# Kernel tuning notes

Hardware: AMD Instinct MI355X
Metric: run time of the kernel (lower is better)

Reference implementation:

```python
import jax, jax.numpy as jnp
import numpy as np

N_EMBD = 1024
N_HEAD = 16
B, T = 4, 2048
NEG = -1e8  # matches the -100000000.0 additive mask in the torch code


def setup_inputs() -> dict:
    key = jax.random.key(0)
    ks = jax.random.split(key, 6)
    x = jax.random.normal(ks[0], (B, T, N_EMBD), dtype=jnp.float32)
    l = jax.random.randint(ks[1], (B,), 1, T + 1, dtype=jnp.int64 if jax.config.jax_enable_x64 else jnp.int32)
    W_attn = jax.random.normal(ks[2], (N_EMBD, 3 * N_EMBD), dtype=jnp.float32) * 0.02
    b_attn = jnp.zeros((3 * N_EMBD,), dtype=jnp.float32)
    W_proj = jax.random.normal(ks[3], (N_EMBD, N_EMBD), dtype=jnp.float32) * 0.02
    b_proj = jnp.zeros((N_EMBD,), dtype=jnp.float32)
    return {"x": x, "l": l, "W_attn": W_attn, "b_attn": b_attn,
            "W_proj": W_proj, "b_proj": b_proj}


def _build_mask(l, Tdim, dtype):
    # additive mask [B, T, T]: 0 where (q < l_b) & (k < l_b) & (k <= q), else NEG
    idx = jnp.arange(Tdim)
    q_ok = idx[None, :, None] < l[:, None, None]
    k_ok = idx[None, None, :] < l[:, None, None]
    causal = idx[:, None] >= idx[None, :]
    keep = q_ok & k_ok & causal[None]
    return jnp.where(keep, jnp.array(0.0, dtype), jnp.array(NEG, dtype))


def reference(x, l, W_attn, b_attn, W_proj, b_proj):
    Bs, Ts, C = x.shape
    H, D = N_HEAD, C // N_HEAD
    qkv = x @ W_attn + b_attn                              # [B,T,3C]
    q, k, v = jnp.split(qkv, 3, axis=-1)
    q = q.reshape(Bs, Ts, H, D).transpose(0, 2, 1, 3)      # [B,H,T,D]
    k = k.reshape(Bs, Ts, H, D).transpose(0, 2, 1, 3)
    v = v.reshape(Bs, Ts, H, D).transpose(0, 2, 1, 3)
    mask = _build_mask(l, Ts, x.dtype)                     # [B,T,T]
    att = jnp.einsum('bhqd,bhkd->bhqk', q, k) * (1.0 / np.sqrt(D))
    att = att + mask[:, None, :, :]
    att = jax.nn.softmax(att, axis=-1)                     # dropout p=0 -> identity
    y = jnp.einsum('bhqk,bhkd->bhqd', att, v)              # [B,H,T,D]
    y = y.transpose(0, 2, 1, 3).reshape(Bs, Ts, C)
    return y @ W_proj + b_proj
```

## Files before the change

### kernel.cpp

```cpp
#include <hip/hip_runtime.h>

typedef unsigned short UST;
typedef __attribute__((ext_vector_type(8))) short short8;
typedef __attribute__((ext_vector_type(4))) float f32x4;

__device__ __forceinline__ UST f2bf(float f) {
  unsigned int u = __float_as_uint(f);
  u += 0x7FFFu + ((u >> 16) & 1u);
  return (UST)(u >> 16);
}
__device__ __forceinline__ float bf2f(UST u) {
  unsigned int x = ((unsigned int)u) << 16;
  return __uint_as_float(x);
}

__device__ __forceinline__ void gload16(const void* g, void* l) {
  __builtin_amdgcn_global_load_lds((__attribute__((address_space(1))) void*)(g),
                                   (__attribute__((address_space(3))) void*)(l), 16, 0, 0);
}

__global__ __launch_bounds__(256) void k_cvt_bf16(const float* __restrict__ X,
                                                  UST* __restrict__ Y, int n8) {
  int i = blockIdx.x * 256 + threadIdx.x;
  if (i >= n8) return;
  const float4* p = (const float4*)(X + (size_t)i * 8);
  float4 a = p[0], b = p[1];
  short8 o;
  o[0] = (short)f2bf(a.x); o[1] = (short)f2bf(a.y);
  o[2] = (short)f2bf(a.z); o[3] = (short)f2bf(a.w);
  o[4] = (short)f2bf(b.x); o[5] = (short)f2bf(b.y);
  o[6] = (short)f2bf(b.z); o[7] = (short)f2bf(b.w);
  *(short8*)(Y + (size_t)i * 8) = o;
}

__global__ __launch_bounds__(256) void k_transpose_bf16(const float* __restrict__ W,
                                                        UST* __restrict__ WT, int K, int N) {
  __shared__ float tile[64][65];
  int n0 = blockIdx.x * 64, k0 = blockIdx.y * 64;
  int t = threadIdx.x;
#pragma unroll
  for (int p = 0; p < 16; ++p) {
    int e = p * 256 + t;
    tile[e >> 6][e & 63] = W[(size_t)(k0 + (e >> 6)) * N + n0 + (e & 63)];
  }
  __syncthreads();
#pragma unroll
  for (int p = 0; p < 16; ++p) {
    int e = p * 256 + t;
    WT[(size_t)(n0 + (e >> 6)) * K + k0 + (e & 63)] = f2bf(tile[e & 63][e >> 6]);
  }
}

template <int EPI, int GX, int GY>
__global__ __launch_bounds__(256) void k_gemm_bt(const UST* __restrict__ A,
                                                 const UST* __restrict__ Bt,
                                                 const float* __restrict__ bias,
                                                 void* __restrict__ Cout,
                                                 int M, int N, int K) {
  __shared__ __align__(16) UST Alds[128 * 32];
  __shared__ __align__(16) UST Blds[128 * 32];
  const int t = threadIdx.x, lane = t & 63, w = t >> 6;
  const int lr = lane & 15, lg = lane >> 4;
  const int f = blockIdx.x;
  const int cpx = (GX * GY) / 8;
  const int swz = (f & 7) * cpx + (f >> 3);
  const int brow = (swz / GX) * 128, bcol = (swz % GX) * 128;
  const int wr = (w >> 1) * 64, wc = (w & 1) * 64;
  f32x4 acc[4][4] = {};

  for (int k0 = 0; k0 < K; k0 += 32) {
#pragma unroll
    for (int j = 0; j < 2; ++j) {
      int c = j * 256 + t;
      gload16(A + (size_t)(brow + (c >> 2)) * K + k0 + (c & 3) * 8,
              &Alds[(j * 256 + w * 64) * 8]);
      gload16(Bt + (size_t)(bcol + (c >> 2)) * K + k0 + (c & 3) * 8,
              &Blds[(j * 256 + w * 64) * 8]);
    }
    __syncthreads();
    short8 af[4], bf[4];
#pragma unroll
    for (int i = 0; i < 4; ++i) {
      af[i] = *(const short8*)&Alds[(wr + i * 16 + lr) * 32 + lg * 8];
      bf[i] = *(const short8*)&Blds[(wc + i * 16 + lr) * 32 + lg * 8];
    }
#pragma unroll
    for (int mi = 0; mi < 4; ++mi)
#pragma unroll
      for (int ni = 0; ni < 4; ++ni)
        acc[mi][ni] = __builtin_amdgcn_mfma_f32_16x16x32_bf16(af[mi], bf[ni], acc[mi][ni], 0, 0, 0);
    __syncthreads();
  }
#pragma unroll
  for (int ni = 0; ni < 4; ++ni) {
    int n = bcol + wc + ni * 16 + lr;
    float bv = bias[n];
#pragma unroll
    for (int mi = 0; mi < 4; ++mi) {
#pragma unroll
      for (int r = 0; r < 4; ++r) {
        int m = brow + wr + mi * 16 + lg * 4 + r;
        float v = acc[mi][ni][r] + bv;
        if (EPI == 1) ((UST*)Cout)[(size_t)m * N + n] = f2bf(v);
        else          ((float*)Cout)[(size_t)m * N + n] = v;
      }
    }
  }
}

__global__ __launch_bounds__(256) void k_vsum(const UST* __restrict__ qkv,
                                              float* __restrict__ pbuf) {
  const int h = blockIdx.x, b = blockIdx.y, z = blockIdx.z;
  const int t = threadIdx.x;
  const int dgrp = t & 7, kslot = t >> 3;
  const UST* Vg = qkv + (size_t)b * 2048 * 3072 + h * 64 + 2048;
  float acc[8] = {0.f, 0.f, 0.f, 0.f, 0.f, 0.f, 0.f, 0.f};
#pragma unroll
  for (int i = 0; i < 16; ++i) {
    int k = z * 512 + kslot * 16 + i;
    short8 v8 = *(const short8*)&Vg[(size_t)k * 3072 + dgrp * 8];
#pragma unroll
    for (int j = 0; j < 8; ++j) acc[j] += bf2f((UST)v8[j]);
  }
  __shared__ float red[32 * 68];
#pragma unroll
  for (int j = 0; j < 8; ++j) red[kslot * 68 + dgrp * 8 + j] = acc[j];
  __syncthreads();
  if (t < 64) {
    float s = 0.f;
#pragma unroll
    for (int ks = 0; ks < 32; ++ks) s += red[ks * 68 + t];
    pbuf[((size_t)(z * 4 + b) * 16 + h) * 64 + t] = s;
  }
}

__global__ __launch_bounds__(256) void k_attn(const UST* __restrict__ qkv,
                                              const int* __restrict__ L,
                                              const float* __restrict__ pbuf,
                                              UST* __restrict__ Ab) {
  const int qt = blockIdx.x, h = blockIdx.y, b = blockIdx.z;
  const int t = threadIdx.x, lane = t & 63, w = t >> 6;
  const int lr = lane & 15, lg = lane >> 4;
  const int lb = L[b];
  const int q0 = qt * 64;
  const int qb = q0 + w * 16;

  const bool need_vm = (lb <= q0 + 63);
  float vm[4];
  if (need_vm) {
    const float* pb = pbuf + ((size_t)b * 16 + h) * 64;
#pragma unroll
    for (int df = 0; df < 4; ++df) {
      int d = df * 16 + lr;
      vm[df] = (pb[d] + pb[4096 + d] + pb[8192 + d] + pb[12288 + d]) * (1.0f / 2048.0f);
    }
  }
  if (q0 >= lb) {
#pragma unroll
    for (int df = 0; df < 4; ++df) {
      UST ov = f2bf(vm[df]);
#pragma unroll
      for (int r = 0; r < 4; ++r) {
        int qrow = qb + lg * 4 + r;
        Ab[(size_t)(b * 2048 + qrow) * 1024 + h * 64 + df * 16 + lr] = ov;
      }
    }
    return;
  }

  const UST* Qg = qkv + (size_t)b * 2048 * 3072 + h * 64;
  const UST* Kg = Qg + 1024;
  const UST* Vg = Qg + 2048;
  __shared__ __align__(16) UST Klds[64 * 64];
  __shared__ __align__(16) UST VT[64 * 64];
  __shared__ __align__(16) UST Plds[4 * 16 * 64];
  UST* Pw = &Plds[w * 16 * 64];

  short8 qf[2];
#pragma unroll
  for (int kk = 0; kk < 2; ++kk)
    qf[kk] = *(const short8*)&Qg[(size_t)(qb + lr) * 3072 + kk * 32 + lg * 8];

  f32x4 o[4] = {};
  float m_run[4], l_run[4];
#pragma unroll
  for (int r = 0; r < 4; ++r) { m_run[r] = -3.0e38f; l_run[r] = 0.f; }

  const int nt = qt + 1;

  for (int kt = 0; kt < nt; ++kt) {
    const int kb = kt * 64;
#pragma unroll
    for (int j = 0; j < 2; ++j) {
      int c = j * 256 + t;
      int row = c >> 3, cc = c & 7;
      gload16(Kg + (size_t)(kb + row) * 3072 + ((cc ^ (row & 7)) * 8),
              &Klds[(j * 256 + w * 64) * 8]);
    }
#pragma unroll
    for (int j = 0; j < 2; ++j) {
      int c = j * 256 + t;
      int key = c & 63, dcc = c >> 6;
      short8 v8 = *(const short8*)&Vg[(size_t)(kb + key) * 3072 + dcc * 8];
#pragma unroll
      for (int jj = 0; jj < 8; ++jj)
        VT[(dcc * 8 + jj) * 64 + (key ^ (jj * 8))] = (UST)v8[jj];
    }
    __syncthreads();

    f32x4 s[4];
#pragma unroll
    for (int kf = 0; kf < 4; ++kf) {
      f32x4 sa = {};
#pragma unroll
      for (int kk = 0; kk < 2; ++kk) {
        short8 kfr = *(const short8*)&Klds[(kf * 16 + lr) * 64 + (((kk * 4 + lg) ^ (lr & 7)) * 8)];
        sa = __builtin_amdgcn_mfma_f32_16x16x32_bf16(qf[kk], kfr, sa, 0, 0, 0);
      }
      s[kf] = sa;
    }
#pragma unroll
    for (int kf = 0; kf < 4; ++kf) {
      int key = kb + kf * 16 + lr;
#pragma unroll
      for (int r = 0; r < 4; ++r) {
        int qrow = qb + lg * 4 + r;
        float mad = (key <= qrow) ? 0.0f : -1e8f;
        s[kf][r] = s[kf][r] * 0.125f + mad;
      }
    }
    float corr[4];
#pragma unroll
    for (int r = 0; r < 4; ++r) {
      float v = fmaxf(fmaxf(s[0][r], s[1][r]), fmaxf(s[2][r], s[3][r]));
      v = fmaxf(v, __shfl_xor(v, 1));
      v = fmaxf(v, __shfl_xor(v, 2));
      v = fmaxf(v, __shfl_xor(v, 4));
      v = fmaxf(v, __shfl_xor(v, 8));
      float mn = fmaxf(m_run[r], v);
      corr[r] = __expf(m_run[r] - mn);
      m_run[r] = mn;
    }
    float rs[4] = {0.f, 0.f, 0.f, 0.f};
#pragma unroll
    for (int kf = 0; kf < 4; ++kf) {
#pragma unroll
      for (int r = 0; r < 4; ++r) {
        float p = __expf(s[kf][r] - m_run[r]);
        s[kf][r] = p;
        rs[r] += p;
      }
    }
#pragma unroll
    for (int r = 0; r < 4; ++r) {
      float v = rs[r];
      v += __shfl_xor(v, 1);
      v += __shfl_xor(v, 2);
      v += __shfl_xor(v, 4);
      v += __shfl_xor(v, 8);
      l_run[r] = l_run[r] * corr[r] + v;
    }
#pragma unroll
    for (int kf = 0; kf < 4; ++kf)
#pragma unroll
      for (int r = 0; r < 4; ++r) {
        int row = lg * 4 + r;
        Pw[row * 64 + ((kf * 16 + lr) ^ ((row & 7) * 8))] = f2bf(s[kf][r]);
      }
#pragma unroll
    for (int df = 0; df < 4; ++df)
#pragma unroll
      for (int r = 0; r < 4; ++r)
        o[df][r] *= corr[r];
#pragma unroll
    for (int kk = 0; kk < 2; ++kk) {
      short8 pf = *(const short8*)&Pw[lr * 64 + ((kk * 32 + lg * 8) ^ ((lr & 7) * 8))];
#pragma unroll
      for (int df = 0; df < 4; ++df) {
        short8 vf = *(const short8*)&VT[(df * 16 + lr) * 64 + (((kk * 4 + lg) ^ (lr & 7)) * 8)];
        o[df] = __builtin_amdgcn_mfma_f32_16x16x32_bf16(pf, vf, o[df], 0, 0, 0);
      }
    }
    __syncthreads();
  }
#pragma unroll
  for (int df = 0; df < 4; ++df) {
#pragma unroll
    for (int r = 0; r < 4; ++r) {
      int qrow = qb + lg * 4 + r;
      float v = (qrow >= lb) ? vm[df] : o[df][r] / l_run[r];
      Ab[(size_t)(b * 2048 + qrow) * 1024 + h * 64 + df * 16 + lr] = f2bf(v);
    }
  }
}

extern "C" void kernel_launch(void* const* d_in, const int* in_sizes, int n_in,
                              void* d_out, int out_size, void* d_ws, size_t ws_size,
                              hipStream_t stream) {
  const float* x  = (const float*)d_in[0];
  const int*   l  = (const int*)d_in[1];
  const float* Wa = (const float*)d_in[2];
  const float* ba = (const float*)d_in[3];
  const float* Wp = (const float*)d_in[4];
  const float* bp = (const float*)d_in[5];

  char* ws = (char*)d_ws;
  UST* xb     = (UST*)(ws);
  UST* WaT    = (UST*)(ws + (16u << 20));
  UST* WpT    = (UST*)(ws + (22u << 20));
  UST* qkvb   = (UST*)(ws + (24u << 20));
  float* pbuf = (float*)(ws + (72u << 20));
  UST* Ab     = xb;

  hipLaunchKernelGGL(k_cvt_bf16, dim3(4096), dim3(256), 0, stream, x, xb, 1048576);
  hipLaunchKernelGGL(k_transpose_bf16, dim3(48, 16), dim3(256), 0, stream, Wa, WaT, 1024, 3072);
  hipLaunchKernelGGL(k_transpose_bf16, dim3(16, 16), dim3(256), 0, stream, Wp, WpT, 1024, 1024);
  hipLaunchKernelGGL((k_gemm_bt<1, 24, 64>), dim3(1536), dim3(256), 0, stream,
                     xb, WaT, ba, (void*)qkvb, 8192, 3072, 1024);
  hipLaunchKernelGGL(k_vsum, dim3(16, 4, 4), dim3(256), 0, stream, qkvb, pbuf);
  hipLaunchKernelGGL(k_attn, dim3(32, 16, 4), dim3(256), 0, stream, qkvb, l, pbuf, Ab);
  hipLaunchKernelGGL((k_gemm_bt<2, 8, 64>), dim3(512), dim3(256), 0, stream,
                     Ab, WpT, bp, d_out, 8192, 1024, 1024);
}
```

Before: 300.3 us.

## Double-buffer K/V tiles in attention and schedule longest query tiles first

The attention kernel now keeps two LDS buffers for the K and V tiles. It prefetches the next K tile asynchronously and loads the next V tile into registers while the current tile is being computed, then writes the transposed V after the PV MFMAs. This cuts the loop to one barrier per iteration and hides global-load latency behind compute. The block index is also reversed so the causal tiles with the most key blocks launch first, which should improve load balance across the grid. The cost is double the LDS for K and V, extra registers to hold the V prefetch, and possibly lower occupancy.

```diff
diff --git a/kernel.cpp b/kernel.cpp
--- a/kernel.cpp
+++ b/kernel.cpp
@@ -138,7 +138,8 @@
                                               const int* __restrict__ L,
                                               const float* __restrict__ pbuf,
                                               UST* __restrict__ Ab) {
-  const int qt = blockIdx.x, h = blockIdx.y, b = blockIdx.z;
+  const int qt = 31 - (int)blockIdx.x;
+  const int h = blockIdx.y, b = blockIdx.z;
   const int t = threadIdx.x, lane = t & 63, w = t >> 6;
   const int lr = lane & 15, lg = lane >> 4;
   const int lb = L[b];
@@ -171,8 +172,8 @@
   const UST* Qg = qkv + (size_t)b * 2048 * 3072 + h * 64;
   const UST* Kg = Qg + 1024;
   const UST* Vg = Qg + 2048;
-  __shared__ __align__(16) UST Klds[64 * 64];
-  __shared__ __align__(16) UST VT[64 * 64];
+  __shared__ __align__(16) UST Klds[2][64 * 64];
+  __shared__ __align__(16) UST VT[2][64 * 64];
   __shared__ __align__(16) UST Plds[4 * 16 * 64];
   UST* Pw = &Plds[w * 16 * 64];
 
@@ -187,34 +188,56 @@
   for (int r = 0; r < 4; ++r) { m_run[r] = -3.0e38f; l_run[r] = 0.f; }
 
   const int nt = qt + 1;
-
-  for (int kt = 0; kt < nt; ++kt) {
-    const int kb = kt * 64;
+  short8 vreg[2];
+
+  auto stageK = [&](int kb, UST* Kb) {
 #pragma unroll
     for (int j = 0; j < 2; ++j) {
       int c = j * 256 + t;
       int row = c >> 3, cc = c & 7;
       gload16(Kg + (size_t)(kb + row) * 3072 + ((cc ^ (row & 7)) * 8),
-              &Klds[(j * 256 + w * 64) * 8]);
-    }
+              &Kb[(j * 256 + w * 64) * 8]);
+    }
+  };
+  auto loadV = [&](int kb) {
+#pragma unroll
+    for (int j = 0; j < 2; ++j) {
+      int c = j * 256 + t;
+      vreg[j] = *(const short8*)&Vg[(size_t)(kb + (c & 63)) * 3072 + (c >> 6) * 8];
+    }
+  };
+  auto writeVT = [&](UST* Vb) {
 #pragma unroll
     for (int j = 0; j < 2; ++j) {
       int c = j * 256 + t;
       int key = c & 63, dcc = c >> 6;
-      short8 v8 = *(const short8*)&Vg[(size_t)(kb + key) * 3072 + dcc * 8];
 #pragma unroll
       for (int jj = 0; jj < 8; ++jj)
-        VT[(dcc * 8 + jj) * 64 + (key ^ (jj * 8))] = (UST)v8[jj];
-    }
-    __syncthreads();
-
+        Vb[(dcc * 8 + jj) * 64 + (key ^ (jj * 8))] = (UST)vreg[j][jj];
+    }
+  };
+
+  stageK(0, Klds[0]);
+  loadV(0);
+  writeVT(VT[0]);
+  __syncthreads();
+
+  for (int kt = 0; kt < nt; ++kt) {
+    const int kb = kt * 64;
+    const int cur = kt & 1;
+    if (kt + 1 < nt) {
+      stageK(kb + 64, Klds[cur ^ 1]);
+      loadV(kb + 64);
+    }
+
+    const UST* Kb = Klds[cur];
     f32x4 s[4];
 #pragma unroll
     for (int kf = 0; kf < 4; ++kf) {
       f32x4 sa = {};
 #pragma unroll
       for (int kk = 0; kk < 2; ++kk) {
-        short8 kfr = *(const short8*)&Klds[(kf * 16 + lr) * 64 + (((kk * 4 + lg) ^ (lr & 7)) * 8)];
+        short8 kfr = *(const short8*)&Kb[(kf * 16 + lr) * 64 + (((kk * 4 + lg) ^ (lr & 7)) * 8)];
         sa = __builtin_amdgcn_mfma_f32_16x16x32_bf16(qf[kk], kfr, sa, 0, 0, 0);
       }
       s[kf] = sa;
@@ -272,15 +295,17 @@
 #pragma unroll
       for (int r = 0; r < 4; ++r)
         o[df][r] *= corr[r];
+    const UST* Vb = VT[cur];
 #pragma unroll
     for (int kk = 0; kk < 2; ++kk) {
       short8 pf = *(const short8*)&Pw[lr * 64 + ((kk * 32 + lg * 8) ^ ((lr & 7) * 8))];
 #pragma unroll
       for (int df = 0; df < 4; ++df) {
-        short8 vf = *(const short8*)&VT[(df * 16 + lr) * 64 + (((kk * 4 + lg) ^ (lr & 7)) * 8)];
+        short8 vf = *(const short8*)&Vb[(df * 16 + lr) * 64 + (((kk * 4 + lg) ^ (lr & 7)) * 8)];
         o[df] = __builtin_amdgcn_mfma_f32_16x16x32_bf16(pf, vf, o[df], 0, 0, 0);
       }
     }
+    if (kt + 1 < nt) writeVT(VT[cur ^ 1]);
     __syncthreads();
   }
 #pragma unroll
```

Result: no change. 295.8 us (-1.5%).
